# Optimization experiments

Hardware: AMD Instinct MI355X
Metric: run time of the kernel (lower is better)

The kernel has to match this reference:

```python
import jax, jax.numpy as jnp
import numpy as np

QUERY_DIM = 1024
CONTEXT_DIM = 1024
HEADS = 8
DIM_HEAD = 64
INNER = HEADS * DIM_HEAD  # 512
SCALE = DIM_HEAD ** -0.5


def setup_inputs() -> dict:
    key = jax.random.key(0)
    ks = jax.random.split(key, 7)
    B, N, M = 2, 2048, 2048
    x = jax.random.normal(ks[0], (B, N, QUERY_DIM), dtype=jnp.float32)
    context = jax.random.normal(ks[1], (B, M, CONTEXT_DIM), dtype=jnp.float32)
    # nn.Linear weights (stored as [out, in] in torch; we use [in, out] here)
    Wq = jax.random.normal(ks[2], (QUERY_DIM, INNER), dtype=jnp.float32) * (QUERY_DIM ** -0.5)
    Wk = jax.random.normal(ks[3], (CONTEXT_DIM, INNER), dtype=jnp.float32) * (CONTEXT_DIM ** -0.5)
    Wv = jax.random.normal(ks[4], (CONTEXT_DIM, INNER), dtype=jnp.float32) * (CONTEXT_DIM ** -0.5)
    Wo = jax.random.normal(ks[5], (INNER, QUERY_DIM), dtype=jnp.float32) * (INNER ** -0.5)
    bo = jax.random.normal(ks[6], (QUERY_DIM,), dtype=jnp.float32) * 0.01
    return {"x": x, "context": context, "Wq": Wq, "Wk": Wk, "Wv": Wv, "Wo": Wo, "bo": bo}


def reference(x, context, Wq, Wk, Wv, Wo, bo):
    B, N, _ = x.shape
    M = context.shape[1]
    # projections (no bias, matching nn.Linear(bias=False))
    q = (x @ Wq).reshape(B, N, HEADS, DIM_HEAD)          # b i h d
    k = (context @ Wk).reshape(B, M, HEADS, DIM_HEAD)    # b j h d
    v = (context @ Wv).reshape(B, M, HEADS, DIM_HEAD)    # b j h d
    # scores in fp32 (ATTN_PRECISION=='fp32' path)
    sim = jnp.einsum('bihd,bjhd->bhij', q.astype(jnp.float32), k.astype(jnp.float32)) * SCALE
    attn = jax.nn.softmax(sim, axis=-1).astype(v.dtype)  # b h i j
    out = jnp.einsum('bhij,bjhd->bihd', attn, v).reshape(B, N, INNER)
    return out @ Wo + bo  # dropout p=0.0 is identity
```

## Files before the change

### kernel.cpp

```cpp
#include <hip/hip_runtime.h>
#include <math.h>

typedef __bf16 bf16_t;
typedef __bf16 bf16x8 __attribute__((ext_vector_type(8)));
typedef __bf16 bf16x4 __attribute__((ext_vector_type(4)));
typedef float  f32x4  __attribute__((ext_vector_type(4)));

#define MFMA16(a, b, c) __builtin_amdgcn_mfma_f32_16x16x32_bf16((a), (b), (c), 0, 0, 0)

#define INNER   512
#define DHEAD   64
#define QSCALE  0.18033688f

__device__ __forceinline__ void g2l(const bf16_t* g, bf16_t* l) {
  __builtin_amdgcn_global_load_lds(
      (const __attribute__((address_space(1))) unsigned int*)g,
      (__attribute__((address_space(3))) unsigned int*)l, 16, 0, 0);
}

#define SBAR0() __builtin_amdgcn_sched_barrier(0)

__global__ __launch_bounds__(256) void pre_w_k(const float* __restrict__ Wq,
                                               const float* __restrict__ Wk,
                                               const float* __restrict__ Wv,
                                               const float* __restrict__ Wo,
                                               bf16_t* __restrict__ WqT,
                                               bf16_t* __restrict__ WkT,
                                               bf16_t* __restrict__ WvT,
                                               bf16_t* __restrict__ WoT) {
  __shared__ float tile[64][65];
  int t = blockIdx.x;
  int z = t >> 7, bid = t & 127;
  const float* W; bf16_t* WT; int K, N;
  if (z == 0)      { W = Wq; WT = WqT; K = 1024; N = 512; }
  else if (z == 1) { W = Wk; WT = WkT; K = 1024; N = 512; }
  else if (z == 2) { W = Wv; WT = WvT; K = 1024; N = 512; }
  else             { W = Wo; WT = WoT; K = 512;  N = 1024; }
  int tK = K >> 6;
  int kt = bid % tK, nt = bid / tK;
  int k0 = kt << 6, n0 = nt << 6;
  for (int idx = threadIdx.x; idx < 4096; idx += 256) {
    int r = idx >> 6, c = idx & 63;
    tile[r][c] = W[(size_t)(k0 + r) * N + n0 + c];
  }
  __syncthreads();
  for (int idx = threadIdx.x; idx < 4096; idx += 256) {
    int r = idx >> 6, c = idx & 63;
    WT[(size_t)(n0 + r) * K + k0 + c] = (bf16_t)tile[c][r];
  }
}

#define QKV_STEP(kc, CURA, NXTA, CURB, NXTB, PRC, PRF)                           \
  {                                                                              \
    asm volatile("s_waitcnt vmcnt(%c0) lgkmcnt(0)" :: "i"(2 * MI) : "memory");   \
    __builtin_amdgcn_s_barrier();                                                \
    SBAR0();                                                                     \
    {                                                                            \
      const int k0b = (((kc) + 1) & (KT - 1)) * 64;                              \
      _Pragma("unroll")                                                          \
      for (int p = 0; p < 4; ++p)                                                \
        g2l(gb + (size_t)(p * 8) * K + k0b, lB + (NXTB) + p * 512);              \
    }                                                                            \
    SBAR0();                \
    {                                                                            \
      const int k0a = (((kc) + 2) & (KT - 1)) * 64;                              \
      _Pragma("unroll")                                                          \
      for (int p = 0; p < MI; ++p) {                                             \
        const float* s_ = ga + (size_t)(p * 8) * K + k0a;                        \
        PRF[2 * p]     = *(const f32x4*)s_;                                      \
        PRF[2 * p + 1] = *(const f32x4*)(s_ + 4);                                \
      }                                                                          \
    }                                                                            \
    SBAR0();                        \
    _Pragma("unroll")                                                            \
    for (int ks = 0; ks < 2; ++ks) {                                             \
      const int phys = ((ks * 4 + quad) ^ (l16 & 7)) << 3;                       \
      bf16x8 af[MI], bfr[4];                                                     \
      _Pragma("unroll")                                                          \
      for (int i = 0; i < MI; ++i)                                               \
        af[i] = *(const bf16x8*)&As[(CURA) + (mrow + i * 16 + l16) * 64 + phys]; \
      _Pragma("unroll")                                                          \
      for (int j = 0; j < 4; ++j)                                                \
        bfr[j] = *(const bf16x8*)&Bs[(CURB) + (ncol + j * 16 + l16) * 64 + phys];\
      _Pragma("unroll")                                                          \
      for (int i = 0; i < MI; ++i)                                               \
        _Pragma("unroll")                                                        \
        for (int j = 0; j < 4; ++j)                                              \
          acc[i][j] = MFMA16(af[i], bfr[j], acc[i][j]);                          \
    }                                                                            \
    asm volatile("s_waitcnt vmcnt(%c0)" :: "i"(2 * MI + 4) : "memory");          \
    SBAR0();                                                                     \
    _Pragma("unroll")                                                            \
    for (int p = 0; p < MI; ++p) {                                               \
      bf16x8 h_;                                                                 \
      _Pragma("unroll")                                                          \
      for (int e = 0; e < 4; ++e) {                                              \
        h_[e]     = (bf16_t)PRC[2 * p][e];                                       \
        h_[4 + e] = (bf16_t)PRC[2 * p + 1][e];                                   \
      }                                                                          \
      *(bf16x8*)&lA[(NXTA) + p * 512 + lane * 8] = h_;                           \
    }                                                                            \
  }

template<int MI>
__device__ __forceinline__ void gemm_qkv_core(bf16_t* sm,
                                              const float* __restrict__ A,
                                              const bf16_t* __restrict__ Bt,
                                              int row0, int n0,
                                              int mode, float scale,
                                              bf16_t* __restrict__ Cb) {
  constexpr int K = 1024, KT = 16;
  constexpr int ABUF = MI * 2048;
  bf16_t* As = sm;
  bf16_t* Bs = sm + 2 * ABUF;
  const int tid = threadIdx.x;
  const int w = tid >> 6, lane = tid & 63, quad = lane >> 4, l16 = lane & 15;
  const int sr8  = lane >> 3;
  const int slog = ((lane & 7) ^ sr8) << 3;
  const float*  ga = A  + (size_t)(row0 + w * (MI * 8) + sr8) * K + slog;
  const bf16_t* gb = Bt + (size_t)(n0   + w * 32 + sr8) * K + slog;
  bf16_t* lA = As + w * MI * 512;
  bf16_t* lB = Bs + w * 2048;

  f32x4 acc[MI][4];
#pragma unroll
  for (int i = 0; i < MI; ++i)
#pragma unroll
    for (int j = 0; j < 4; ++j) acc[i][j] = f32x4{0.f, 0.f, 0.f, 0.f};

  f32x4 pA0[2 * MI], pA1[2 * MI];
  const int mrow = (w & 1) * (MI * 16), ncol = (w >> 1) << 6;

#pragma unroll
  for (int p = 0; p < MI; ++p) {
    const float* s = ga + (size_t)(p * 8) * K;
    f32x4 f0 = *(const f32x4*)s;
    f32x4 f1 = *(const f32x4*)(s + 4);
    bf16x8 h;
#pragma unroll
    for (int e = 0; e < 4; ++e) { h[e] = (bf16_t)f0[e]; h[4 + e] = (bf16_t)f1[e]; }
    *(bf16x8*)&lA[p * 512 + lane * 8] = h;
  }
  SBAR0();
#pragma unroll
  for (int p = 0; p < 4; ++p)
    g2l(gb + (size_t)(p * 8) * K, lB + p * 512);
  SBAR0();
#pragma unroll
  for (int p = 0; p < MI; ++p) {
    const float* s = ga + (size_t)(p * 8) * K + 64;
    pA0[2 * p]     = *(const f32x4*)s;
    pA0[2 * p + 1] = *(const f32x4*)(s + 4);
  }
  SBAR0();

  for (int kc = 0; kc < KT; kc += 2) {
    QKV_STEP(kc,     0,    ABUF, 0,    8192, pA0, pA1);
    QKV_STEP(kc + 1, ABUF, 0,    8192, 0,    pA1, pA0);
  }

#pragma unroll
  for (int i = 0; i < MI; ++i) {
    int row = row0 + mrow + i * 16 + quad * 4;
#pragma unroll
    for (int j = 0; j < 4; ++j) {
      int col = n0 + ncol + j * 16 + l16;
      if (mode == 2) {
        int bb = row >> 11, key = row & 2047;
        int hh = col >> 6,  d   = col & 63;
        bf16x4 v = { (bf16_t)acc[i][j][0], (bf16_t)acc[i][j][1],
                     (bf16_t)acc[i][j][2], (bf16_t)acc[i][j][3] };
        *(bf16x4*)&Cb[((size_t)((bb * 8 + hh) * 64 + d)) * 2048 + key] = v;
      } else {
#pragma unroll
        for (int r = 0; r < 4; ++r)
          Cb[(size_t)(row + r) * 512 + col] = (bf16_t)(acc[i][j][r] * scale);
      }
    }
  }
}

__global__ __launch_bounds__(256, 2) void gemm_qkv_k(const float* __restrict__ x,
                                                     const float* __restrict__ ctx,
                                                     const bf16_t* __restrict__ WqT,
                                                     const bf16_t* __restrict__ WkT,
                                                     const bf16_t* __restrict__ WvT,
                                                     bf16_t* __restrict__ Qb,
                                                     bf16_t* __restrict__ Kb,
                                                     bf16_t* __restrict__ Vt) {
  __shared__ __align__(16) bf16_t smem[32768];
  int bid = blockIdx.x;
  if (bid < 256) {
    int z = bid >> 7;
    int t = bid & 127;
    int xcd = t & 7, slot = t >> 3;
    int m = (xcd << 2) | (slot >> 2);
    int n = slot & 3;
    const float* A   = (z == 0) ? x   : ctx;
    const bf16_t* Bt = (z == 0) ? WqT : WkT;
    bf16_t* C        = (z == 0) ? Qb  : Kb;
    float scale      = (z == 0) ? QSCALE : 1.0f;
    gemm_qkv_core<4>(smem, A, Bt, m * 128, n * 128, 0, scale, C);
  } else {
    int t = bid - 256;
    int xcd = t & 7, slot = t >> 3;
    int m = (xcd << 3) | (slot >> 2);
    int n = slot & 3;
    gemm_qkv_core<2>(smem, ctx, WvT, m * 64, n * 128, 2, 1.0f, Vt);
  }
}

template<int BM>
__device__ __forceinline__ void gemm_core(const bf16_t* __restrict__ Ab,
                                          const bf16_t* __restrict__ Bt,
                                          int K, int N, int row0, int n0,
                                          float* __restrict__ Cf,
                                          const float* __restrict__ bias) {
  constexpr int MI = BM / 32;
  __shared__ bf16_t As[2 * BM * 64];
  __shared__ bf16_t Bs[2 * 128 * 64];
  const int tid = threadIdx.x;
  const int w = tid >> 6, lane = tid & 63, quad = lane >> 4, l16 = lane & 15;

  const int sr8  = lane >> 3;
  const int slog = ((lane & 7) ^ sr8) << 3;
  const bf16_t* ga = Ab + (size_t)(row0 + w * (BM / 4) + sr8) * K + slog;
  const bf16_t* gb = Bt + (size_t)(n0   + w * 32 + sr8) * K + slog;
  bf16_t* lA = As + w * (BM / 4) * 64;
  bf16_t* lB = Bs + w * 2048;

  f32x4 acc[MI][4];
#pragma unroll
  for (int i = 0; i < MI; ++i)
#pragma unroll
    for (int j = 0; j < 4; ++j) acc[i][j] = f32x4{0.f, 0.f, 0.f, 0.f};

  const int mrow = (w & 1) * (BM / 2), ncol = (w >> 1) << 6;
  const int KT = K >> 6;

#pragma unroll
  for (int p = 0; p < MI; ++p)
    g2l(ga + (size_t)(p * 8) * K, lA + p * 512);
#pragma unroll
  for (int p = 0; p < 4; ++p)
    g2l(gb + (size_t)(p * 8) * K, lB + p * 512);

  for (int kc = 0; kc < KT; ++kc) {
    const int curA = (kc & 1) * (BM * 64), nxtA = ((kc + 1) & 1) * (BM * 64);
    const int curB = (kc & 1) * 8192,      nxtB = ((kc + 1) & 1) * 8192;
    __syncthreads();
    if (kc + 1 < KT) {
      const int k0 = (kc + 1) * 64;
#pragma unroll
      for (int p = 0; p < MI; ++p)
        g2l(ga + (size_t)(p * 8) * K + k0, lA + nxtA + p * 512);
#pragma unroll
      for (int p = 0; p < 4; ++p)
        g2l(gb + (size_t)(p * 8) * K + k0, lB + nxtB + p * 512);
    }
#pragma unroll
    for (int ks = 0; ks < 2; ++ks) {
      const int phys = ((ks * 4 + quad) ^ (l16 & 7)) << 3;
      bf16x8 af[MI], bfr[4];
#pragma unroll
      for (int i = 0; i < MI; ++i)
        af[i] = *(const bf16x8*)&As[curA + (mrow + i * 16 + l16) * 64 + phys];
#pragma unroll
      for (int j = 0; j < 4; ++j)
        bfr[j] = *(const bf16x8*)&Bs[curB + (ncol + j * 16 + l16) * 64 + phys];
#pragma unroll
      for (int i = 0; i < MI; ++i)
#pragma unroll
        for (int j = 0; j < 4; ++j)
          acc[i][j] = MFMA16(af[i], bfr[j], acc[i][j]);
    }
  }

#pragma unroll
  for (int i = 0; i < MI; ++i) {
    int row = row0 + mrow + i * 16 + quad * 4;
#pragma unroll
    for (int j = 0; j < 4; ++j) {
      int col = n0 + ncol + j * 16 + l16;
#pragma unroll
      for (int r = 0; r < 4; ++r)
        Cf[(size_t)(row + r) * N + col] = acc[i][j][r] + bias[col];
    }
  }
}

__global__ __launch_bounds__(256, 2) void gemm_out_k(const bf16_t* __restrict__ AO,
                                                     const bf16_t* __restrict__ WoT,
                                                     const float* __restrict__ bo,
                                                     float* __restrict__ out) {
  int bid = blockIdx.x;
  int xcd  = bid & 7;
  int slot = bid >> 3;
  int m = (xcd << 3) | (slot >> 3);
  int n = slot & 7;
  gemm_core<64>(AO, WoT, 512, 1024, m * 64, n * 128, out, bo);
}

__global__ __launch_bounds__(256, 2) void attn_k(const bf16_t* __restrict__ Qb,
                                                 const bf16_t* __restrict__ Kb,
                                                 const bf16_t* __restrict__ Vt,
                                                 bf16_t* __restrict__ AO) {
  const int tid = threadIdx.x;
  const int w = tid >> 6, lane = tid & 63, quad = lane >> 4, l16 = lane & 15;
  int bid = blockIdx.x;
  int xcd  = bid & 7;
  int slot = bid >> 3;
  const int qt = slot & 31;
  const int bh = (xcd << 1) | (slot >> 5);
  const int b = bh >> 3, h = bh & 7;

  __shared__ bf16_t Ks[2 * 128 * 64];
  __shared__ bf16_t Vs[64 * 128];
  __shared__ bf16_t Ps[64 * 136];

  const int qrow = b * 2048 + qt * 64 + w * 16 + l16;
  const bf16_t* qptr = Qb + (size_t)qrow * INNER + h * DHEAD;
  bf16x8 bq[2];
  bq[0] = *(const bf16x8*)(qptr + quad * 8);
  bq[1] = *(const bf16x8*)(qptr + 32 + quad * 8);

  f32x4 o[4];
#pragma unroll
  for (int dt = 0; dt < 4; ++dt) o[dt] = f32x4{0.f, 0.f, 0.f, 0.f};
  float m_s = -__builtin_inff(), l_s = 0.f;

  const bf16_t* kbase  = Kb + ((size_t)b * 2048) * INNER + h * DHEAD;
  const bf16_t* vtbase = Vt + ((size_t)bh * 64) * 2048;

  const int krow = lane >> 3;
  const int kcol = ((lane & 7) ^ (lane >> 3)) << 3;
  const int vrow = lane >> 4;

#pragma unroll
  for (int p = 0; p < 4; ++p)
    g2l(kbase + (size_t)(w * 32 + p * 8 + krow) * INNER + kcol,
        &Ks[w * 2048 + p * 512]);

  for (int kt = 0; kt < 16; ++kt) {
    const int cur = (kt & 1) * 8192, nxt = ((kt + 1) & 1) * 8192;
    __syncthreads();
#pragma unroll
    for (int p = 0; p < 4; ++p) {
      int vlog = ((lane & 15) ^ ((p * 4 + vrow) & 15)) << 3;
      g2l(vtbase + (size_t)(w * 16 + p * 4 + vrow) * 2048 + kt * 128 + vlog,
          &Vs[w * 2048 + p * 512]);
    }
    SBAR0();
    {
      const int ktn = (kt + 1) & 15;
#pragma unroll
      for (int p = 0; p < 4; ++p)
        g2l(kbase + (size_t)(ktn * 128 + w * 32 + p * 8 + krow) * INNER + kcol,
            &Ks[nxt + w * 2048 + p * 512]);
    }
    SBAR0();

    f32x4 s[8];
#pragma unroll
    for (int jt = 0; jt < 8; ++jt) s[jt] = f32x4{0.f, 0.f, 0.f, 0.f};
    __builtin_amdgcn_s_setprio(1);
#pragma unroll
    for (int jt = 0; jt < 8; ++jt) {
#pragma unroll
      for (int ks = 0; ks < 2; ++ks) {
        int phys = ((ks * 4 + quad) ^ (l16 & 7)) << 3;
        bf16x8 ak = *(const bf16x8*)&Ks[cur + (jt * 16 + l16) * 64 + phys];
        s[jt] = MFMA16(ak, bq[ks], s[jt]);
      }
    }
    __builtin_amdgcn_s_setprio(0);

    float mx = -__builtin_inff();
#pragma unroll
    for (int jt = 0; jt < 8; ++jt) {
      float a = fmaxf(fmaxf(s[jt][0], s[jt][1]), fmaxf(s[jt][2], s[jt][3]));
      mx = fmaxf(mx, a);
    }
    mx = fmaxf(mx, __shfl_xor(mx, 16, 64));
    mx = fmaxf(mx, __shfl_xor(mx, 32, 64));
    float mnew = fmaxf(m_s, mx);
    float alpha = __builtin_amdgcn_exp2f(m_s - mnew);
    float rs = 0.f;
#pragma unroll
    for (int jt = 0; jt < 8; ++jt) {
#pragma unroll
      for (int r = 0; r < 4; ++r) {
        float p = __builtin_amdgcn_exp2f(s[jt][r] - mnew);
        s[jt][r] = p;
        rs += p;
      }
    }
    rs += __shfl_xor(rs, 16, 64);
    rs += __shfl_xor(rs, 32, 64);
    l_s = l_s * alpha + rs;
    m_s = mnew;
#pragma unroll
    for (int dt = 0; dt < 4; ++dt) o[dt] *= alpha;

#pragma unroll
    for (int jt = 0; jt < 8; ++jt) {
      bf16x4 pk = { (bf16_t)s[jt][0], (bf16_t)s[jt][1],
                    (bf16_t)s[jt][2], (bf16_t)s[jt][3] };
      *(bf16x4*)&Ps[(w * 16 + l16) * 136 + jt * 16 + quad * 4] = pk;
    }

    asm volatile("s_waitcnt vmcnt(4) lgkmcnt(0)" ::: "memory");
    __builtin_amdgcn_s_barrier();
    SBAR0();

    __builtin_amdgcn_s_setprio(1);
#pragma unroll
    for (int kc = 0; kc < 4; ++kc) {
      bf16x8 bp = *(const bf16x8*)&Ps[(w * 16 + l16) * 136 + kc * 32 + quad * 8];
#pragma unroll
      for (int dt = 0; dt < 4; ++dt) {
        int phys = ((kc * 4 + quad) ^ l16) << 3;
        bf16x8 av = *(const bf16x8*)&Vs[(dt * 16 + l16) * 128 + phys];
        o[dt] = MFMA16(av, bp, o[dt]);
      }
    }
    __builtin_amdgcn_s_setprio(0);
  }

  float inv = 1.0f / l_s;
#pragma unroll
  for (int dt = 0; dt < 4; ++dt) {
    bf16x4 ov = { (bf16_t)(o[dt][0] * inv), (bf16_t)(o[dt][1] * inv),
                  (bf16_t)(o[dt][2] * inv), (bf16_t)(o[dt][3] * inv) };
    *(bf16x4*)&Ps[(w * 16 + l16) * 136 + dt * 16 + quad * 4] = ov;
  }
  __syncthreads();
  {
    int sr = tid >> 2, sc = (tid & 3) << 4;
    int4 r0 = *(const int4*)&Ps[sr * 136 + sc];
    int4 r1 = *(const int4*)&Ps[sr * 136 + sc + 8];
    bf16_t* aout = AO + ((size_t)(b * 2048 + qt * 64 + sr)) * INNER + h * DHEAD + sc;
    *(int4*)aout       = r0;
    *(int4*)(aout + 8) = r1;
  }
}

extern "C" void kernel_launch(void* const* d_in, const int* in_sizes, int n_in,
                              void* d_out, int out_size, void* d_ws, size_t ws_size,
                              hipStream_t stream) {
  const float* x   = (const float*)d_in[0];
  const float* ctx = (const float*)d_in[1];
  const float* Wq  = (const float*)d_in[2];
  const float* Wk  = (const float*)d_in[3];
  const float* Wv  = (const float*)d_in[4];
  const float* Wo  = (const float*)d_in[5];
  const float* bo  = (const float*)d_in[6];
  float* out = (float*)d_out;

  char* ws = (char*)d_ws;
  const size_t MB = 1048576;
  bf16_t* WqT = (bf16_t*)(ws + 0 * MB);
  bf16_t* WkT = (bf16_t*)(ws + 1 * MB);
  bf16_t* WvT = (bf16_t*)(ws + 2 * MB);
  bf16_t* WoT = (bf16_t*)(ws + 3 * MB);
  bf16_t* Qb  = (bf16_t*)(ws + 4 * MB);
  bf16_t* Kb  = (bf16_t*)(ws + 8 * MB);
  bf16_t* Vt  = (bf16_t*)(ws + 12 * MB);
  bf16_t* AO  = (bf16_t*)(ws + 16 * MB);

  pre_w_k<<<512, 256, 0, stream>>>(Wq, Wk, Wv, Wo, WqT, WkT, WvT, WoT);
  gemm_qkv_k<<<512, 256, 0, stream>>>(x, ctx, WqT, WkT, WvT, Qb, Kb, Vt);
  attn_k<<<512, 256, 0, stream>>>(Qb, Kb, Vt, AO);
  gemm_out_k<<<512, 256, 0, stream>>>(AO, WoT, bo, out);
}
```

Measured before the change: 159.3 us.

## Triple-buffer output GEMM loads and add lazy softmax rescaling in attention

The output projection GEMM is specialised for K=512 and moves from double to triple LDS buffering, prefetching two tiles ahead with explicit vmcnt waits, so each iteration needs one barrier instead of a full syncthreads. The attention kernel skips the running-max update and the rescaling of the output accumulator unless some lane's max has grown by more than 8 (in log2 units). The first change aims to hide global load latency. The second removes exp and multiply work in most iterations, at the cost of letting exponents reach up to 2^8 before a rescale, which could affect precision. The triple buffer also raises LDS use.

New measurement: 158.9 us. Within noise of the previous version (-0.2%).

```diff
diff --git a/kernel.cpp b/kernel.cpp
--- a/kernel.cpp
+++ b/kernel.cpp
@@ -210,81 +210,90 @@
   }
 }
 
-template<int BM>
-__device__ __forceinline__ void gemm_core(const bf16_t* __restrict__ Ab,
-                                          const bf16_t* __restrict__ Bt,
-                                          int K, int N, int row0, int n0,
-                                          float* __restrict__ Cf,
-                                          const float* __restrict__ bias) {
-  constexpr int MI = BM / 32;
-  __shared__ bf16_t As[2 * BM * 64];
-  __shared__ bf16_t Bs[2 * 128 * 64];
+__device__ __forceinline__ void gemm_out_core(const bf16_t* __restrict__ Ab,
+                                              const bf16_t* __restrict__ Bt,
+                                              int row0, int n0,
+                                              float* __restrict__ Cf,
+                                              const float* __restrict__ bias) {
+  constexpr int K = 512, KT = 8;
+  __shared__ bf16_t As[3 * 4096];
+  __shared__ bf16_t Bs[3 * 8192];
   const int tid = threadIdx.x;
   const int w = tid >> 6, lane = tid & 63, quad = lane >> 4, l16 = lane & 15;
-
   const int sr8  = lane >> 3;
   const int slog = ((lane & 7) ^ sr8) << 3;
-  const bf16_t* ga = Ab + (size_t)(row0 + w * (BM / 4) + sr8) * K + slog;
+  const bf16_t* ga = Ab + (size_t)(row0 + w * 16 + sr8) * K + slog;
   const bf16_t* gb = Bt + (size_t)(n0   + w * 32 + sr8) * K + slog;
-  bf16_t* lA = As + w * (BM / 4) * 64;
+  bf16_t* lA = As + w * 1024;
   bf16_t* lB = Bs + w * 2048;
 
-  f32x4 acc[MI][4];
-#pragma unroll
-  for (int i = 0; i < MI; ++i)
+  f32x4 acc[2][4];
+#pragma unroll
+  for (int i = 0; i < 2; ++i)
 #pragma unroll
     for (int j = 0; j < 4; ++j) acc[i][j] = f32x4{0.f, 0.f, 0.f, 0.f};
 
-  const int mrow = (w & 1) * (BM / 2), ncol = (w >> 1) << 6;
-  const int KT = K >> 6;
-
-#pragma unroll
-  for (int p = 0; p < MI; ++p)
-    g2l(ga + (size_t)(p * 8) * K, lA + p * 512);
-#pragma unroll
-  for (int p = 0; p < 4; ++p)
-    g2l(gb + (size_t)(p * 8) * K, lB + p * 512);
-
+  const int mrow = (w & 1) * 32, ncol = (w >> 1) << 6;
+
+#pragma unroll
+  for (int t = 0; t < 2; ++t) {
+#pragma unroll
+    for (int p = 0; p < 2; ++p)
+      g2l(ga + (size_t)(p * 8) * K + t * 64, lA + t * 4096 + p * 512);
+    SBAR0();
+#pragma unroll
+    for (int p = 0; p < 4; ++p)
+      g2l(gb + (size_t)(p * 8) * K + t * 64, lB + t * 8192 + p * 512);
+    SBAR0();
+  }
+
+  int rbuf = 0;
+  int wbuf = 2;
   for (int kc = 0; kc < KT; ++kc) {
-    const int curA = (kc & 1) * (BM * 64), nxtA = ((kc + 1) & 1) * (BM * 64);
-    const int curB = (kc & 1) * 8192,      nxtB = ((kc + 1) & 1) * 8192;
-    __syncthreads();
-    if (kc + 1 < KT) {
-      const int k0 = (kc + 1) * 64;
-#pragma unroll
-      for (int p = 0; p < MI; ++p)
-        g2l(ga + (size_t)(p * 8) * K + k0, lA + nxtA + p * 512);
+    asm volatile("s_waitcnt vmcnt(6) lgkmcnt(0)" ::: "memory");
+    __builtin_amdgcn_s_barrier();
+    SBAR0();
+    {
+      const int kn = ((kc + 2) & (KT - 1)) * 64;
+#pragma unroll
+      for (int p = 0; p < 2; ++p)
+        g2l(ga + (size_t)(p * 8) * K + kn, lA + wbuf * 4096 + p * 512);
+      SBAR0();
 #pragma unroll
       for (int p = 0; p < 4; ++p)
-        g2l(gb + (size_t)(p * 8) * K + k0, lB + nxtB + p * 512);
-    }
+        g2l(gb + (size_t)(p * 8) * K + kn, lB + wbuf * 8192 + p * 512);
+      SBAR0();
+    }
+    const int cA = rbuf * 4096, cB = rbuf * 8192;
 #pragma unroll
     for (int ks = 0; ks < 2; ++ks) {
       const int phys = ((ks * 4 + quad) ^ (l16 & 7)) << 3;
-      bf16x8 af[MI], bfr[4];
-#pragma unroll
-      for (int i = 0; i < MI; ++i)
-        af[i] = *(const bf16x8*)&As[curA + (mrow + i * 16 + l16) * 64 + phys];
+      bf16x8 af[2], bfr[4];
+#pragma unroll
+      for (int i = 0; i < 2; ++i)
+        af[i] = *(const bf16x8*)&As[cA + (mrow + i * 16 + l16) * 64 + phys];
 #pragma unroll
       for (int j = 0; j < 4; ++j)
-        bfr[j] = *(const bf16x8*)&Bs[curB + (ncol + j * 16 + l16) * 64 + phys];
-#pragma unroll
-      for (int i = 0; i < MI; ++i)
+        bfr[j] = *(const bf16x8*)&Bs[cB + (ncol + j * 16 + l16) * 64 + phys];
+#pragma unroll
+      for (int i = 0; i < 2; ++i)
 #pragma unroll
         for (int j = 0; j < 4; ++j)
           acc[i][j] = MFMA16(af[i], bfr[j], acc[i][j]);
     }
-  }
-
-#pragma unroll
-  for (int i = 0; i < MI; ++i) {
+    rbuf = (rbuf == 2) ? 0 : rbuf + 1;
+    wbuf = (wbuf == 2) ? 0 : wbuf + 1;
+  }
+
+#pragma unroll
+  for (int i = 0; i < 2; ++i) {
     int row = row0 + mrow + i * 16 + quad * 4;
 #pragma unroll
     for (int j = 0; j < 4; ++j) {
       int col = n0 + ncol + j * 16 + l16;
 #pragma unroll
       for (int r = 0; r < 4; ++r)
-        Cf[(size_t)(row + r) * N + col] = acc[i][j][r] + bias[col];
+        Cf[(size_t)(row + r) * 1024 + col] = acc[i][j][r] + bias[col];
     }
   }
 }
@@ -298,7 +307,7 @@
   int slot = bid >> 3;
   int m = (xcd << 3) | (slot >> 3);
   int n = slot & 7;
-  gemm_core<64>(AO, WoT, 512, 1024, m * 64, n * 128, out, bo);
+  gemm_out_core(AO, WoT, m * 64, n * 128, out, bo);
 }
 
 __global__ __launch_bounds__(256, 2) void attn_k(const bf16_t* __restrict__ Qb,
@@ -383,24 +392,27 @@
     }
     mx = fmaxf(mx, __shfl_xor(mx, 16, 64));
     mx = fmaxf(mx, __shfl_xor(mx, 32, 64));
-    float mnew = fmaxf(m_s, mx);
-    float alpha = __builtin_amdgcn_exp2f(m_s - mnew);
+    if (!__all(mx - m_s <= 8.0f)) {
+      float mnew = fmaxf(m_s, mx);
+      float alpha = __builtin_amdgcn_exp2f(m_s - mnew);
+      l_s *= alpha;
+#pragma unroll
+      for (int dt = 0; dt < 4; ++dt) o[dt] *= alpha;
+      m_s = mnew;
+    }
     float rs = 0.f;
 #pragma unroll
     for (int jt = 0; jt < 8; ++jt) {
 #pragma unroll
       for (int r = 0; r < 4; ++r) {
-        float p = __builtin_amdgcn_exp2f(s[jt][r] - mnew);
+        float p = __builtin_amdgcn_exp2f(s[jt][r] - m_s);
         s[jt][r] = p;
         rs += p;
       }
     }
     rs += __shfl_xor(rs, 16, 64);
     rs += __shfl_xor(rs, 32, 64);
-    l_s = l_s * alpha + rs;
-    m_s = mnew;
-#pragma unroll
-    for (int dt = 0; dt < 4; ++dt) o[dt] *= alpha;
+    l_s += rs;
 
 #pragma unroll
     for (int jt = 0; jt < 8; ++jt) {
```
